# Performance work log

Hardware: AMD Instinct MI355X
Metric: run time of the kernel (lower is better)

The kernel has to match this reference:

```python
import jax, jax.numpy as jnp
import numpy as np
import math

B, D, S, C, H = 8192, 512, 5, 2048, 4

def setup_inputs() -> dict:
    key = jax.random.key(0)
    ks = jax.random.split(key, 8)
    return {
        "features": jax.random.normal(ks[0], (B, D), dtype=jnp.float32),
        "logits": jax.random.normal(ks[1], (S, B, C), dtype=jnp.float32),
        "scale_feats": jax.random.normal(ks[2], (S, B, D), dtype=jnp.float32),
        "Wq": jax.random.normal(ks[3], (D, D), dtype=jnp.float32) * 0.02,
        "bq": jnp.zeros((D,), jnp.float32),
        "Wk": jax.random.normal(ks[4], (D, D), dtype=jnp.float32) * 0.02,
        "bk": jnp.zeros((D,), jnp.float32),
        "Wv": jax.random.normal(ks[5], (D, D), dtype=jnp.float32) * 0.02,
        "bv": jnp.zeros((D,), jnp.float32),
        "scale_emb": jax.random.normal(ks[6], (S, D), dtype=jnp.float32) * 0.02,
        "temperature": jnp.float32(0.07),
        "attn_w": jnp.ones((3,), jnp.float32) / 3.0,
    }

def reference(features, logits, scale_feats, Wq, bq, Wk, bk, Wv, bv, scale_emb, temperature, attn_w):
    b, d = features.shape
    s = scale_feats.shape[0]
    hd = d // H
    t = jnp.abs(temperature)

    # ---- multihead attention over scales (V is computed in torch but unused) ----
    Q = (features @ Wq + bq).reshape(b, H, hd)                      # [B,H,hd]
    sf_emb = scale_feats + scale_emb[:, None, :]                    # [S,B,D]
    K = (sf_emb @ Wk + bk).reshape(s, b, H, hd)                     # [S,B,H,hd]
    scores = jnp.einsum('bhd,sbhd->bhs', Q, K) / jnp.float32(math.sqrt(hd))
    attn_mha = jax.nn.softmax(scores / t, axis=-1).mean(axis=1)     # [B,S]

    # ---- geometric (angular) attention ----
    fn = features / jnp.linalg.norm(features, axis=-1, keepdims=True).clip(1e-12)
    sfn = scale_feats / jnp.linalg.norm(scale_feats, axis=-1, keepdims=True).clip(1e-12)
    cos_sim = jnp.einsum('bd,sbd->bs', fn, sfn)                     # [B,S]
    angles = jnp.arccos(jnp.clip(cos_sim, -1.0 + 1e-7, 1.0 - 1e-7))
    attn_geo = jax.nn.softmax(jnp.exp(-angles / t), axis=-1)        # [B,S]

    # ---- Cayley-Menger volume-proxy attention ----
    # simplex points: [features, scale_feat, cos(a)*f + sin(a)*s for a in {pi/4, pi/2, 3pi/4}]
    c = jnp.float32(math.sqrt(0.5))
    cf = jnp.array([1.0, 0.0, c, 0.0, -c], jnp.float32)             # coeffs on features
    cs = jnp.array([0.0, 1.0, c, 1.0, c], jnp.float32)              # coeffs on scale_feat
    simplex = (cf[None, :, None, None] * features[None, None] +
               cs[None, :, None, None] * scale_feats[:, None])      # [S,5,B,D]
    norms = jnp.sum(simplex * simplex, axis=-1)                     # [S,5,B]
    gram = jnp.einsum('spbd,sqbd->spqb', simplex, simplex)          # [S,5,5,B]
    distsq = norms[:, :, None] + norms[:, None, :] - 2.0 * gram     # [S,5,5,B]
    volumes = distsq.mean(axis=(1, 2)).T                            # [B,S]
    attn_cay = jax.nn.softmax(volumes / t, axis=-1)

    # ---- fuse attention types ----
    w = jax.nn.softmax(attn_w, axis=0)
    combined = w[0] * attn_mha + w[1] * attn_geo + w[2] * attn_cay  # [B,S]
    combined = combined / combined.sum(axis=-1, keepdims=True)

    combined_logits = jnp.einsum('bs,sbc->bc', combined, logits)    # [B,C]
    return (combined_logits, combined)
```

## Files before the change

### kernel.cpp

```cpp
#include <hip/hip_runtime.h>
#include <math.h>

#define B_N 8192
#define D_N 512
#define S_N 5
#define C_N 2048
#define H_N 4
#define RB 16

typedef __attribute__((ext_vector_type(8))) short bf16x8;
typedef __attribute__((ext_vector_type(4))) float floatx4;

__device__ __forceinline__ float bf2f(short u) {
  union { unsigned int i; float f; } c;
  c.i = ((unsigned int)(unsigned short)u) << 16;
  return c.f;
}
__device__ __forceinline__ short f2bf(float f) {
  union { float f; unsigned int i; } c; c.f = f;
  unsigned int x = c.i;
  x += 0x7fffu + ((x >> 16) & 1u);
  return (short)(x >> 16);
}
__device__ __forceinline__ unsigned long long pack4(float a, float b, float c, float d) {
  return (unsigned long long)(unsigned short)f2bf(a)
       | ((unsigned long long)(unsigned short)f2bf(b) << 16)
       | ((unsigned long long)(unsigned short)f2bf(c) << 32)
       | ((unsigned long long)(unsigned short)f2bf(d) << 48);
}

__global__ __launch_bounds__(256) void k_prep(const float* __restrict__ Wq,
                                              const float* __restrict__ Wk,
                                              short* __restrict__ WqT,
                                              short* __restrict__ Wkb) {
  __shared__ float lds[64][65];
  const int bx = blockIdx.x, t = threadIdx.x;
  if (bx < 64) {
    const int r0 = (bx >> 3) * 64, c0 = (bx & 7) * 64;
#pragma unroll
    for (int i = 0; i < 16; ++i) {
      int r = i * 4 + (t >> 6), c = t & 63;
      lds[r][c] = Wq[(size_t)(r0 + r) * 512 + c0 + c];
    }
    __syncthreads();
#pragma unroll
    for (int i = 0; i < 16; ++i) {
      int cL = i * 4 + (t >> 6), rL = t & 63;
      WqT[(size_t)(c0 + cL) * 512 + r0 + rL] = f2bf(lds[rL][cL]);
    }
  } else {
    const int base = (bx - 64) * 8192 + t * 4;
#pragma unroll
    for (int i = 0; i < 8; ++i) {
      int idx = base + i * 1024;
      floatx4 v = *(const floatx4*)(Wk + idx);
      *(unsigned long long*)(Wkb + idx) = pack4(v[0], v[1], v[2], v[3]);
    }
  }
}

__global__ __launch_bounds__(256, 2) void k_mega(
    const float* __restrict__ f, const float* __restrict__ sf,
    const float* __restrict__ emb, const short* __restrict__ WqT,
    const short* __restrict__ Wkb, const float* __restrict__ bq,
    const float* __restrict__ bk, const float* __restrict__ logits,
    const float* __restrict__ temp, const float* __restrict__ attn_w,
    float* __restrict__ out, float* __restrict__ comb_out) {
  __shared__ __align__(16) float fLds[RB * 512];
  __shared__ __align__(16) short Qbf[RB * 512];
  __shared__ __align__(16) short sfe[S_N * RB * 132];
  __shared__ float ffLds[RB];
  __shared__ float qtLds[RB][H_N];
  __shared__ float scLds[RB][H_N][S_N];
  __shared__ float fsLds[S_N][RB];
  __shared__ float ssLds[S_N][RB];
  __shared__ float combLds[RB][S_N];

  const int tid = threadIdx.x;
  const int lane = tid & 63;
  const int wid = tid >> 6;
  const int b0 = blockIdx.x * RB;
  const floatx4 fz = {0.f, 0.f, 0.f, 0.f};

  {
    const int r0 = tid >> 4;
    const int c0 = (tid & 15) * 32;
    const float* fp = f + (size_t)(b0 + r0) * D_N + c0;
    char* fb = (char*)fLds;
    float ffp = 0.0f;
#pragma unroll
    for (int i = 0; i < 8; ++i) {
      floatx4 v = *(const floatx4*)(fp + i * 4);
      ffp += v[0]*v[0] + v[1]*v[1] + v[2]*v[2] + v[3]*v[3];
      int bo = (r0 * 2048 + (c0 + i * 4) * 4) ^ ((r0 & 7) << 4);
      *(floatx4*)(fb + bo) = v;
    }
    ffp += __shfl_xor(ffp, 1, 64);
    ffp += __shfl_xor(ffp, 2, 64);
    ffp += __shfl_xor(ffp, 4, 64);
    ffp += __shfl_xor(ffp, 8, 64);
    if ((tid & 15) == 0) ffLds[r0] = ffp;
  }
  __syncthreads();

  {
    const int wcol0 = wid * 128;
    floatx4 acc[8];
#pragma unroll
    for (int n = 0; n < 8; ++n) acc[n] = fz;
    const char* fb = (const char*)fLds;
    const int row = lane & 15;

    for (int ks = 0; ks < 16; ++ks) {
      bf16x8 bfr[8];
#pragma unroll
      for (int n = 0; n < 8; ++n) {
        int col = wcol0 + n * 16 + (lane & 15);
        bfr[n] = *(const bf16x8*)(WqT + (size_t)col * 512 + ks * 32 + (lane >> 4) * 8);
      }
      int kbase = ks * 32 + (lane >> 4) * 8;
      int bo0 = (row * 2048 + kbase * 4) ^ ((row & 7) << 4);
      int bo1 = (row * 2048 + kbase * 4 + 16) ^ ((row & 7) << 4);
      floatx4 a0 = *(const floatx4*)(fb + bo0);
      floatx4 a1 = *(const floatx4*)(fb + bo1);
      bf16x8 afr;
      afr[0] = f2bf(a0[0]); afr[1] = f2bf(a0[1]); afr[2] = f2bf(a0[2]); afr[3] = f2bf(a0[3]);
      afr[4] = f2bf(a1[0]); afr[5] = f2bf(a1[1]); afr[6] = f2bf(a1[2]); afr[7] = f2bf(a1[3]);
#pragma unroll
      for (int n = 0; n < 8; ++n)
        acc[n] = __builtin_amdgcn_mfma_f32_16x16x32_bf16(afr, bfr[n], acc[n], 0, 0, 0);
    }

    float bqv[8], bkv[8];
#pragma unroll
    for (int n = 0; n < 8; ++n) {
      int col = wcol0 + n * 16 + (lane & 15);
      bqv[n] = bq[col];
      bkv[n] = bk[col];
    }
#pragma unroll
    for (int j = 0; j < 4; ++j) {
      int orow = (lane >> 4) * 4 + j;
      float qp = 0.0f;
#pragma unroll
      for (int n = 0; n < 8; ++n) {
        float qv = acc[n][j] + bqv[n];
        int col = wcol0 + n * 16 + (lane & 15);
        int bo = (orow * 1024 + col * 2) ^ ((orow & 7) << 4);
        *(short*)((char*)Qbf + bo) = f2bf(qv);
        qp += qv * bkv[n];
      }
      qp += __shfl_xor(qp, 1, 64);
      qp += __shfl_xor(qp, 2, 64);
      qp += __shfl_xor(qp, 4, 64);
      qp += __shfl_xor(qp, 8, 64);
      if ((lane & 15) == 0) qtLds[orow][wid] = qp;
    }
  }
  __syncthreads();

  float scp[S_N][4];
#pragma unroll
  for (int s = 0; s < S_N; ++s)
#pragma unroll
    for (int j = 0; j < 4; ++j) scp[s][j] = 0.0f;
  float ssp[S_N] = {0, 0, 0, 0, 0}, fsp[S_N] = {0, 0, 0, 0, 0};

  const int h = wid;
  for (int cc = 0; cc < 4; ++cc) {
    {
      const int r1 = tid >> 4;
      const int cs0 = (tid & 15) * 8;
      const int ac0 = cc * 128 + cs0;
      const char* fb = (const char*)fLds;
      int bo0 = (r1 * 2048 + ac0 * 4) ^ ((r1 & 7) << 4);
      int bo1 = (r1 * 2048 + ac0 * 4 + 16) ^ ((r1 & 7) << 4);
      floatx4 f0 = *(const floatx4*)(fb + bo0);
      floatx4 f1 = *(const floatx4*)(fb + bo1);
      float fv[8] = {f0[0], f0[1], f0[2], f0[3], f1[0], f1[1], f1[2], f1[3]};
#pragma unroll
      for (int s = 0; s < S_N; ++s) {
        const float* sp = sf + ((size_t)s * B_N + b0 + r1) * D_N + ac0;
        floatx4 s0 = *(const floatx4*)(sp);
        floatx4 s1 = *(const floatx4*)(sp + 4);
        const float* ep = emb + s * D_N + ac0;
        floatx4 e0 = *(const floatx4*)(ep);
        floatx4 e1 = *(const floatx4*)(ep + 4);
        float sv[8] = {s0[0], s0[1], s0[2], s0[3], s1[0], s1[1], s1[2], s1[3]};
        float se[8] = {s0[0]+e0[0], s0[1]+e0[1], s0[2]+e0[2], s0[3]+e0[3],
                       s1[0]+e1[0], s1[1]+e1[1], s1[2]+e1[2], s1[3]+e1[3]};
        float ssl = 0.0f, fsl = 0.0f;
#pragma unroll
        for (int q = 0; q < 8; ++q) { ssl += sv[q] * sv[q]; fsl += fv[q] * sv[q]; }
        ssp[s] += ssl; fsp[s] += fsl;
        int rowbase = (s * RB + r1) * 264 + cs0 * 2;
        *(unsigned long long*)((char*)sfe + rowbase)     = pack4(se[0], se[1], se[2], se[3]);
        *(unsigned long long*)((char*)sfe + rowbase + 8) = pack4(se[4], se[5], se[6], se[7]);
      }
    }
    __syncthreads();

    {
      floatx4 acc2[8];
#pragma unroll
      for (int n = 0; n < 8; ++n) acc2[n] = fz;
      const int row = lane & 15;
#pragma unroll
      for (int ks = 0; ks < 4; ++ks) {
        bf16x8 bfr[8];
#pragma unroll
        for (int n = 0; n < 8; ++n) {
          int a = cc * 128 + n * 16 + (lane & 15);
          bfr[n] = *(const bf16x8*)(Wkb + (size_t)a * 512 + h * 128 + ks * 32 + (lane >> 4) * 8);
        }
        int bo = (row * 1024 + (h * 128 + ks * 32 + (lane >> 4) * 8) * 2) ^ ((row & 7) << 4);
        bf16x8 afr = *(const bf16x8*)((const char*)Qbf + bo);
#pragma unroll
        for (int n = 0; n < 8; ++n)
          acc2[n] = __builtin_amdgcn_mfma_f32_16x16x32_bf16(afr, bfr[n], acc2[n], 0, 0, 0);
      }
#pragma unroll
      for (int s = 0; s < S_N; ++s) {
#pragma unroll
        for (int j = 0; j < 4; ++j) {
          int orow = (lane >> 4) * 4 + j;
          int base = (s * RB + orow) * 264 + (lane & 15) * 2;
          float p = 0.0f;
#pragma unroll
          for (int n = 0; n < 8; ++n) {
            short svv = *(const short*)((const char*)sfe + base + n * 32);
            p += acc2[n][j] * bf2f(svv);
          }
          scp[s][j] += p;
        }
      }
    }
    __syncthreads();
  }

#pragma unroll
  for (int s = 0; s < S_N; ++s)
#pragma unroll
    for (int j = 0; j < 4; ++j) {
      float v = scp[s][j];
      v += __shfl_xor(v, 1, 64);
      v += __shfl_xor(v, 2, 64);
      v += __shfl_xor(v, 4, 64);
      v += __shfl_xor(v, 8, 64);
      if ((lane & 15) == 0) scLds[(lane >> 4) * 4 + j][wid][s] = v;
    }
  {
    const int r1 = tid >> 4;
#pragma unroll
    for (int s = 0; s < S_N; ++s) {
      float u = ssp[s], v = fsp[s];
      u += __shfl_xor(u, 1, 64); v += __shfl_xor(v, 1, 64);
      u += __shfl_xor(u, 2, 64); v += __shfl_xor(v, 2, 64);
      u += __shfl_xor(u, 4, 64); v += __shfl_xor(v, 4, 64);
      u += __shfl_xor(u, 8, 64); v += __shfl_xor(v, 8, 64);
      if ((tid & 15) == 0) { ssLds[s][r1] = u; fsLds[s][r1] = v; }
    }
  }
  __syncthreads();

  if (tid < RB) {
    const int r = tid;
    const float ffv = ffLds[r];
    const float t = fabsf(temp[0]);

    float amha[S_N] = {0, 0, 0, 0, 0};
    const float inv_mha = 1.0f / (sqrtf(128.0f) * t);
#pragma unroll
    for (int hh = 0; hh < H_N; ++hh) {
      float lg[S_N];
#pragma unroll
      for (int s = 0; s < S_N; ++s) lg[s] = (scLds[r][hh][s] + qtLds[r][hh]) * inv_mha;
      float mx = lg[0];
#pragma unroll
      for (int s = 1; s < S_N; ++s) mx = fmaxf(mx, lg[s]);
      float e[S_N], sum = 0;
#pragma unroll
      for (int s = 0; s < S_N; ++s) { e[s] = __expf(lg[s] - mx); sum += e[s]; }
      float isum = 0.25f / sum;
#pragma unroll
      for (int s = 0; s < S_N; ++s) amha[s] += e[s] * isum;
    }

    float ageo[S_N];
    {
      const float nf = fmaxf(sqrtf(ffv), 1e-12f);
      float g[S_N];
#pragma unroll
      for (int s = 0; s < S_N; ++s) {
        float ns = fmaxf(sqrtf(ssLds[s][r]), 1e-12f);
        float cs0 = fsLds[s][r] / (nf * ns);
        cs0 = fminf(fmaxf(cs0, -1.0f + 1e-7f), 1.0f - 1e-7f);
        g[s] = __expf(-acosf(cs0) / t);
      }
      float mx = g[0];
#pragma unroll
      for (int s = 1; s < S_N; ++s) mx = fmaxf(mx, g[s]);
      float sum = 0;
#pragma unroll
      for (int s = 0; s < S_N; ++s) { ageo[s] = __expf(g[s] - mx); sum += ageo[s]; }
#pragma unroll
      for (int s = 0; s < S_N; ++s) ageo[s] /= sum;
    }

    float acay[S_N];
    {
      const float SQ2 = 1.41421356237309515f;
      const float Aff = 0.72f;
      const float Ass = 0.72f - 0.32f * SQ2;
      const float Afs = -(8.0f + 4.0f * SQ2) / 25.0f;
      float lg[S_N];
#pragma unroll
      for (int s = 0; s < S_N; ++s)
        lg[s] = (Aff * ffv + Ass * ssLds[s][r] + Afs * fsLds[s][r]) / t;
      float mx = lg[0];
#pragma unroll
      for (int s = 1; s < S_N; ++s) mx = fmaxf(mx, lg[s]);
      float sum = 0;
#pragma unroll
      for (int s = 0; s < S_N; ++s) { acay[s] = __expf(lg[s] - mx); sum += acay[s]; }
#pragma unroll
      for (int s = 0; s < S_N; ++s) acay[s] /= sum;
    }

    float w0 = attn_w[0], w1 = attn_w[1], w2 = attn_w[2];
    float wm = fmaxf(w0, fmaxf(w1, w2));
    float e0 = __expf(w0 - wm), e1 = __expf(w1 - wm), e2 = __expf(w2 - wm);
    float wsum = e0 + e1 + e2;
    w0 = e0 / wsum; w1 = e1 / wsum; w2 = e2 / wsum;

    float cb[S_N], csum = 0;
#pragma unroll
    for (int s = 0; s < S_N; ++s) {
      cb[s] = w0 * amha[s] + w1 * ageo[s] + w2 * acay[s];
      csum += cb[s];
    }
    float ic = 1.0f / csum;
#pragma unroll
    for (int s = 0; s < S_N; ++s) {
      float cv = cb[s] * ic;
      combLds[r][s] = cv;
      comb_out[(size_t)(b0 + r) * S_N + s] = cv;
    }
  }
  __syncthreads();

  {
    const int c0 = tid * 8;
#pragma unroll 2
    for (int r = 0; r < RB; r += 2) {
      float cA[S_N], cB[S_N];
#pragma unroll
      for (int s = 0; s < S_N; ++s) { cA[s] = combLds[r][s]; cB[s] = combLds[r + 1][s]; }
      floatx4 aA = fz, aB = fz, bA = fz, bB = fz;
#pragma unroll
      for (int s = 0; s < S_N; ++s) {
        const float* lpA = logits + ((size_t)s * B_N + b0 + r) * C_N + c0;
        floatx4 xA0 = *(const floatx4*)(lpA);
        floatx4 xA1 = *(const floatx4*)(lpA + 4);
        floatx4 xB0 = *(const floatx4*)(lpA + C_N);
        floatx4 xB1 = *(const floatx4*)(lpA + C_N + 4);
        aA += xA0 * cA[s]; aB += xA1 * cA[s];
        bA += xB0 * cB[s]; bB += xB1 * cB[s];
      }
      float* opA = out + (size_t)(b0 + r) * C_N + c0;
      *(floatx4*)(opA) = aA;
      *(floatx4*)(opA + 4) = aB;
      *(floatx4*)(opA + C_N) = bA;
      *(floatx4*)(opA + C_N + 4) = bB;
    }
  }
}

extern "C" void kernel_launch(void* const* d_in, const int* in_sizes, int n_in,
                              void* d_out, int out_size, void* d_ws, size_t ws_size,
                              hipStream_t stream) {
  const float* features = (const float*)d_in[0];
  const float* logits   = (const float*)d_in[1];
  const float* sf       = (const float*)d_in[2];
  const float* Wq       = (const float*)d_in[3];
  const float* bq       = (const float*)d_in[4];
  const float* Wk       = (const float*)d_in[5];
  const float* bk       = (const float*)d_in[6];
  const float* emb      = (const float*)d_in[9];
  const float* temp     = (const float*)d_in[10];
  const float* attn_w   = (const float*)d_in[11];

  float* out  = (float*)d_out;
  float* comb = out + (size_t)B_N * C_N;

  char* w = (char*)d_ws;
  short* WqT = (short*)(w);
  short* Wkb = (short*)(w + 524288);

  k_prep<<<dim3(96), dim3(256), 0, stream>>>(Wq, Wk, WqT, Wkb);
  k_mega<<<dim3(512), dim3(256), 0, stream>>>(features, sf, emb, WqT, Wkb, bq, bk,
                                              logits, temp, attn_w, out, comb);
}
```

Measured before the change: 169.7 us.

## Split logits mixing out of fused kernel into separate high-parallelism kernel

Moves the combined-weight logits mixing (streaming 5x8192x2048 floats) out of the mega kernel into a new kernel with one block per batch row. The mega kernel now only writes the combined weights, and the new kernel re-reads them from global memory. The aim is to run the bandwidth-bound mixing phase at full occupancy instead of inside the register/LDS-heavy mega kernel with only 512 blocks. The cost is an extra launch and a small round trip through global memory.

```diff
diff --git a/kernel.cpp b/kernel.cpp
--- a/kernel.cpp
+++ b/kernel.cpp
@@ -63,9 +63,8 @@
     const float* __restrict__ f, const float* __restrict__ sf,
     const float* __restrict__ emb, const short* __restrict__ WqT,
     const short* __restrict__ Wkb, const float* __restrict__ bq,
-    const float* __restrict__ bk, const float* __restrict__ logits,
-    const float* __restrict__ temp, const float* __restrict__ attn_w,
-    float* __restrict__ out, float* __restrict__ comb_out) {
+    const float* __restrict__ bk, const float* __restrict__ temp,
+    const float* __restrict__ attn_w, float* __restrict__ comb_out) {
   __shared__ __align__(16) float fLds[RB * 512];
   __shared__ __align__(16) short Qbf[RB * 512];
   __shared__ __align__(16) short sfe[S_N * RB * 132];
@@ -74,7 +73,6 @@
   __shared__ float scLds[RB][H_N][S_N];
   __shared__ float fsLds[S_N][RB];
   __shared__ float ssLds[S_N][RB];
-  __shared__ float combLds[RB][S_N];
 
   const int tid = threadIdx.x;
   const int lane = tid & 63;
@@ -341,39 +339,30 @@
     }
     float ic = 1.0f / csum;
 #pragma unroll
-    for (int s = 0; s < S_N; ++s) {
-      float cv = cb[s] * ic;
-      combLds[r][s] = cv;
-      comb_out[(size_t)(b0 + r) * S_N + s] = cv;
-    }
-  }
-  __syncthreads();
-
-  {
-    const int c0 = tid * 8;
-#pragma unroll 2
-    for (int r = 0; r < RB; r += 2) {
-      float cA[S_N], cB[S_N];
-#pragma unroll
-      for (int s = 0; s < S_N; ++s) { cA[s] = combLds[r][s]; cB[s] = combLds[r + 1][s]; }
-      floatx4 aA = fz, aB = fz, bA = fz, bB = fz;
-#pragma unroll
-      for (int s = 0; s < S_N; ++s) {
-        const float* lpA = logits + ((size_t)s * B_N + b0 + r) * C_N + c0;
-        floatx4 xA0 = *(const floatx4*)(lpA);
-        floatx4 xA1 = *(const floatx4*)(lpA + 4);
-        floatx4 xB0 = *(const floatx4*)(lpA + C_N);
-        floatx4 xB1 = *(const floatx4*)(lpA + C_N + 4);
-        aA += xA0 * cA[s]; aB += xA1 * cA[s];
-        bA += xB0 * cB[s]; bB += xB1 * cB[s];
-      }
-      float* opA = out + (size_t)(b0 + r) * C_N + c0;
-      *(floatx4*)(opA) = aA;
-      *(floatx4*)(opA + 4) = aB;
-      *(floatx4*)(opA + C_N) = bA;
-      *(floatx4*)(opA + C_N + 4) = bB;
-    }
-  }
+    for (int s = 0; s < S_N; ++s) comb_out[(size_t)(b0 + r) * S_N + s] = cb[s] * ic;
+  }
+}
+
+__global__ __launch_bounds__(256) void k_mix(const float* __restrict__ logits,
+                                             const float* __restrict__ comb,
+                                             float* __restrict__ out) {
+  const int b = blockIdx.x;
+  const int c0 = threadIdx.x * 8;
+  float cs[S_N];
+#pragma unroll
+  for (int s = 0; s < S_N; ++s) cs[s] = comb[(size_t)b * S_N + s];
+  floatx4 accA = {0, 0, 0, 0}, accB = {0, 0, 0, 0};
+#pragma unroll
+  for (int s = 0; s < S_N; ++s) {
+    const float* lp = logits + ((size_t)s * B_N + b) * C_N + c0;
+    floatx4 lA = *(const floatx4*)lp;
+    floatx4 lB = *(const floatx4*)(lp + 4);
+    accA += lA * cs[s];
+    accB += lB * cs[s];
+  }
+  float* op = out + (size_t)b * C_N + c0;
+  *(floatx4*)op = accA;
+  *(floatx4*)(op + 4) = accB;
 }
 
 extern "C" void kernel_launch(void* const* d_in, const int* in_sizes, int n_in,
@@ -399,5 +388,6 @@
 
   k_prep<<<dim3(96), dim3(256), 0, stream>>>(Wq, Wk, WqT, Wkb);
   k_mega<<<dim3(512), dim3(256), 0, stream>>>(features, sf, emb, WqT, Wkb, bq, bk,
-                                              logits, temp, attn_w, out, comb);
-}
+                                              temp, attn_w, comb);
+  k_mix<<<dim3(8192), dim3(256), 0, stream>>>(logits, comb, out);
+}
```

New measurement: 169.9 us. About the same (+0.1%).
